# Kernel optimization log

Hardware: AMD Instinct MI355X
Metric: run time of the kernel (lower is better)

## Reference

```python
import jax, jax.numpy as jnp
import numpy as np

# Multi-scale schedule for (T,H,W)=(1,16,16) from get_latent2scale_schedule
SCHEDULE = [(1, 1, 1), (1, 2, 2), (1, 3, 3), (1, 4, 4), (1, 5, 5),
            (1, 6, 6), (1, 8, 8), (1, 10, 10), (1, 13, 13), (1, 16, 16)]

N_EMBED = 196560  # Leech lattice kissing number
EMBED_DIM = 24


def _resize(x, thw):
    # x: [B, D, T, H, W] -> [B, D, t, h, w] (trilinear/bilinear interpolation)
    b, d = x.shape[:2]
    return jax.image.resize(x, (b, d) + tuple(thw), method='bilinear')


def _quantize(r, codebook):
    """SphericalVectorQuantizer with predefined (pre-normalized) codebook.
    r: [B, D, t, h, w].  d = -z @ codebook^T; argmin(d) == argmax(sim)."""
    b, d = r.shape[0], r.shape[1]
    spatial = r.shape[2:]
    zf = jnp.moveaxis(r, 1, -1).reshape(-1, d)            # [N, D] tokens
    sim = zf @ codebook.T                                  # [N, K] cosine similarity
    idx = jnp.argmax(jax.lax.stop_gradient(sim), axis=1)   # argmin of -sim
    zq = codebook[idx]                                     # gather [N, D]
    zq = zq / jnp.linalg.norm(zq, axis=-1, keepdims=True)  # F.normalize (no-op if unit)
    zq = zf + jax.lax.stop_gradient(zq - zf)               # straight-through estimator
    zq = jnp.moveaxis(zq.reshape((b,) + spatial + (d,)), -1, 1)
    return zq, idx


def setup_inputs() -> dict:
    key = jax.random.key(0)
    k1, k2 = jax.random.split(key)
    z = jax.random.normal(k1, (2, 24, 1, 16, 16), jnp.float32)
    cb = jax.random.normal(k2, (N_EMBED, EMBED_DIM), jnp.float32)
    cb = cb / jnp.linalg.norm(cb, axis=-1, keepdims=True)  # normalized Leech codebook
    return {"z": z, "codebook": cb}


def reference(z, codebook):
    # Multi-scale residual quantization (Algorithm 1, RQ-style):
    # downsample residual -> spherical VQ (STE) -> upsample -> accumulate/subtract.
    B, D, T, H, W = z.shape
    residual = z
    z_hat = jnp.zeros_like(z)
    all_idx = []
    for thw in SCHEDULE:
        r_down = _resize(residual, thw)
        zq, idx = _quantize(r_down, codebook)
        zq_up = _resize(zq, (T, H, W))
        z_hat = z_hat + zq_up
        residual = residual - jax.lax.stop_gradient(zq_up)  # residual detach (default)
        all_idx.append(idx)
    indices = jnp.concatenate(all_idx)  # [B * sum(t*h*w)] int codes
    return z_hat, indices
```

## Files before the change

kernel.cpp:

```cpp
#include <hip/hip_runtime.h>
#include <stdint.h>

#define KCB 196560
#define DIM 24
#define BB  2
#define ZEL 12288
#define NRB 384
#define RBS 512

typedef __attribute__((ext_vector_type(8)))  __bf16 bf16x8;
typedef __attribute__((ext_vector_type(16))) float  f32x16;

__device__ __forceinline__ unsigned long long pack_key(float sim, int idx) {
  unsigned u = __float_as_uint(sim);
  u = (u & 0x80000000u) ? ~u : (u | 0x80000000u);
  return ((unsigned long long)u << 32) | (unsigned)(~(unsigned)idx);
}

__global__ __launch_bounds__(256) void init_kernel(const float* __restrict__ z,
    float* __restrict__ residual, float* __restrict__ out, float* __restrict__ rdown,
    ushort* __restrict__ th, ushort* __restrict__ tl, int outTotal) {
  __shared__ float plane[256];
  int tid = threadIdx.x;
  int e = blockIdx.x * 256 + tid;
  if (e < outTotal) out[e] = 0.0f;
  if (blockIdx.x < 48) {
    float v = z[e];
    residual[e] = v;
    plane[tid] = v;
    __syncthreads();
    if (tid == 0) {
      int t = 1;
      float inv_scale = 16.0f / (float)t;
      float ks = inv_scale;
      float sf_h = (0.0f + 0.5f) * inv_scale - 0.5f;
      float sf_w = (0.0f + 0.5f) * inv_scale - 0.5f;
      float wh[16], ww[16];
      float sh = 0.f, sw = 0.f;
#pragma unroll
      for (int i = 0; i < 16; ++i) {
        float vh = fmaxf(0.f, 1.f - fabsf(sf_h - (float)i) / ks);
        wh[i] = vh; sh += vh;
        float vw = fmaxf(0.f, 1.f - fabsf(sf_w - (float)i) / ks);
        ww[i] = vw; sw += vw;
      }
#pragma unroll
      for (int i = 0; i < 16; ++i) { wh[i] /= sh; ww[i] /= sw; }
      float acc = 0.f;
      for (int ih = 0; ih < 16; ++ih) {
        float ra = 0.f;
#pragma unroll
        for (int iw = 0; iw < 16; ++iw) ra = fmaf(ww[iw], plane[ih * 16 + iw], ra);
        acc = fmaf(wh[ih], ra, acc);
      }
      int b = blockIdx.x / DIM, d = blockIdx.x - (blockIdx.x / DIM) * DIM;
      int token = b;
      rdown[token * DIM + d] = acc;
      unsigned bits = __float_as_uint(acc);
      float hif = __uint_as_float(bits & 0xffff0000u);
      th[token * DIM + d] = (ushort)(bits >> 16);
      tl[token * DIM + d] = (ushort)(__float_as_uint(acc - hif) >> 16);
    }
  }
}

__global__ __launch_bounds__(256) void cbprep_kernel(const float* __restrict__ cb,
    ushort* __restrict__ ch, ushort* __restrict__ cl) {
  int j = blockIdx.x * 256 + threadIdx.x;
  if (j >= KCB * 6) return;
  int row = j / 6, q = j - row * 6;
  float4 v = *(const float4*)(cb + (size_t)row * 24 + q * 4);
  float xs[4] = {v.x, v.y, v.z, v.w};
  unsigned h[4], l[4];
#pragma unroll
  for (int k = 0; k < 4; ++k) {
    unsigned bits = __float_as_uint(xs[k]);
    h[k] = bits >> 16;
    float hif = __uint_as_float(bits & 0xffff0000u);
    l[k] = __float_as_uint(xs[k] - hif) >> 16;
  }
  *(uint2*)(ch + (size_t)row * 24 + q * 4) = make_uint2(h[0] | (h[1] << 16), h[2] | (h[3] << 16));
  *(uint2*)(cl + (size_t)row * 24 + q * 4) = make_uint2(l[0] | (l[1] << 16), l[2] | (l[3] << 16));
}

__global__ __launch_bounds__(256) void score_kernel(const ushort* __restrict__ ch,
    const ushort* __restrict__ cl, const ushort* __restrict__ th,
    const ushort* __restrict__ tl, float* __restrict__ blockmax, int T) {
  const int bx = blockIdx.x;
  const int rb = bx % NRB, tb = bx / NRB;
  const int tid = threadIdx.x, lane = tid & 63, wv = tid >> 6;
  const int col = lane & 31, g = lane >> 5;
  const int tbase = tb * 128;
  const int ntt = min(4, (T - tbase + 31) >> 5);
  const uint4 z4 = make_uint4(0, 0, 0, 0);

  bf16x8 bh[4][2], bl[4][2];
#pragma unroll
  for (int tt = 0; tt < 4; ++tt) {
    int token = tbase + tt * 32 + col;
    bool tv = (tt < ntt) && (token < T);
    const ushort* tr = th + (size_t)token * 24;
    const ushort* sr = tl + (size_t)token * 24;
    uint4 h0 = tv ? *(const uint4*)(tr + g * 8) : z4;
    uint4 h1 = (tv && g == 0) ? *(const uint4*)(tr + 16) : z4;
    uint4 l0 = tv ? *(const uint4*)(sr + g * 8) : z4;
    uint4 l1 = (tv && g == 0) ? *(const uint4*)(sr + 16) : z4;
    bh[tt][0] = __builtin_bit_cast(bf16x8, h0);
    bh[tt][1] = __builtin_bit_cast(bf16x8, h1);
    bl[tt][0] = __builtin_bit_cast(bf16x8, l0);
    bl[tt][1] = __builtin_bit_cast(bf16x8, l1);
  }

  const f32x16 fzero = {};
  float runmax[4] = {-3.402823466e38f, -3.402823466e38f, -3.402823466e38f, -3.402823466e38f};
  const int rbase = rb * RBS + wv * 128;

#pragma unroll
  for (int rt = 0; rt < 4; ++rt) {
    int tilebase = rbase + rt * 32;
    if (tilebase >= KCB) continue;
    int row = tilebase + col;
    bool rv = row < KCB;
    const ushort* cr = ch + (size_t)row * 24;
    const ushort* dr = cl + (size_t)row * 24;
    uint4 a0 = rv ? *(const uint4*)(cr + g * 8) : z4;
    uint4 a1 = (rv && g == 0) ? *(const uint4*)(cr + 16) : z4;
    uint4 c0 = rv ? *(const uint4*)(dr + g * 8) : z4;
    uint4 c1 = (rv && g == 0) ? *(const uint4*)(dr + 16) : z4;
    bf16x8 ah0 = __builtin_bit_cast(bf16x8, a0);
    bf16x8 ah1 = __builtin_bit_cast(bf16x8, a1);
    bf16x8 al0 = __builtin_bit_cast(bf16x8, c0);
    bf16x8 al1 = __builtin_bit_cast(bf16x8, c1);
    int limit = KCB - tilebase;
    bool full = limit >= 32;
#pragma unroll
    for (int tt = 0; tt < 4; ++tt) {
      if (tt >= ntt) continue;
      f32x16 acc = __builtin_amdgcn_mfma_f32_32x32x16_bf16(ah0, bh[tt][0], fzero, 0, 0, 0);
      acc = __builtin_amdgcn_mfma_f32_32x32x16_bf16(ah1, bh[tt][1], acc, 0, 0, 0);
      acc = __builtin_amdgcn_mfma_f32_32x32x16_bf16(al0, bh[tt][0], acc, 0, 0, 0);
      acc = __builtin_amdgcn_mfma_f32_32x32x16_bf16(al1, bh[tt][1], acc, 0, 0, 0);
      acc = __builtin_amdgcn_mfma_f32_32x32x16_bf16(ah0, bl[tt][0], acc, 0, 0, 0);
      acc = __builtin_amdgcn_mfma_f32_32x32x16_bf16(ah1, bl[tt][1], acc, 0, 0, 0);
      float m;
      if (full) {
        float m01 = fmaxf(acc[0], acc[1]),  m23 = fmaxf(acc[2], acc[3]);
        float m45 = fmaxf(acc[4], acc[5]),  m67 = fmaxf(acc[6], acc[7]);
        float m89 = fmaxf(acc[8], acc[9]),  mab = fmaxf(acc[10], acc[11]);
        float mcd = fmaxf(acc[12], acc[13]), mef = fmaxf(acc[14], acc[15]);
        m = fmaxf(fmaxf(fmaxf(m01, m23), fmaxf(m45, m67)),
                  fmaxf(fmaxf(m89, mab), fmaxf(mcd, mef)));
      } else {
        m = -3.402823466e38f;
#pragma unroll
        for (int r = 0; r < 16; ++r) {
          int rowid = (r & 3) + 8 * (r >> 2) + 4 * g;
          if (rowid < limit) m = fmaxf(m, acc[r]);
        }
      }
      runmax[tt] = fmaxf(runmax[tt], m);
    }
  }

  __shared__ float lmax[4][4][32];
#pragma unroll
  for (int tt = 0; tt < 4; ++tt) {
    float v = fmaxf(runmax[tt], __shfl_xor(runmax[tt], 32));
    if (lane < 32) lmax[wv][tt][col] = v;
  }
  __syncthreads();
  if (tid < 128) {
    int tt = tid >> 5, c = tid & 31;
    if (tt < ntt) {
      float m = fmaxf(fmaxf(lmax[0][tt][c], lmax[1][tt][c]),
                      fmaxf(lmax[2][tt][c], lmax[3][tt][c]));
      int token = tbase + tt * 32 + c;
      if (token < T) blockmax[token * NRB + rb] = m;
    }
  }
}

__global__ __launch_bounds__(256) void finalize_kernel(const float* __restrict__ cb,
    const float* __restrict__ rdown, const float* __restrict__ blockmax,
    unsigned long long* __restrict__ best, int T) {
  int tid = threadIdx.x, lane = tid & 63, wv = tid >> 6;
  int tok = blockIdx.x * 4 + wv;
  if (tok >= T) return;

  float x = (lane < DIM) ? rdown[tok * DIM + lane] : 0.f;
  float av[DIM];
#pragma unroll
  for (int k = 0; k < DIM; ++k)
    av[k] = __uint_as_float(__builtin_amdgcn_readlane(__float_as_uint(x), k));
  float ss = 0.f;
#pragma unroll
  for (int k = 0; k < DIM; ++k) ss = fmaf(av[k], av[k], ss);
  float eps = 1e-3f * sqrtf(ss) + 1e-30f;

  const float* bmrow = blockmax + (size_t)tok * NRB;
  float bv[6];
#pragma unroll
  for (int i = 0; i < 6; ++i) bv[i] = bmrow[lane + 64 * i];
  float M = fmaxf(fmaxf(fmaxf(bv[0], bv[1]), fmaxf(bv[2], bv[3])), fmaxf(bv[4], bv[5]));
#pragma unroll
  for (int d = 32; d; d >>= 1) M = fmaxf(M, __shfl_xor(M, d));
  float thr = M - eps;

  unsigned long long bk = 0ull;
#pragma unroll
  for (int i = 0; i < 6; ++i) {
    unsigned long long mask = __ballot(bv[i] >= thr);
    while (mask) {
      int l = __ffsll((unsigned long long)mask) - 1;
      mask &= mask - 1;
      int rowb = (l + 64 * i) * RBS;
      for (int r8 = 0; r8 < 8; ++r8) {
        int row = rowb + r8 * 64 + lane;
        if (row < KCB) {
          const float* cv = cb + (size_t)row * DIM;
          float acc = 0.f;
#pragma unroll
          for (int k = 0; k < DIM; ++k) acc = fmaf(av[k], cv[k], acc);
          unsigned long long key = pack_key(acc, row);
          if (key > bk) bk = key;
        }
      }
    }
  }
#pragma unroll
  for (int d = 32; d; d >>= 1) {
    unsigned long long o = __shfl_xor(bk, d);
    if (o > bk) bk = o;
  }
  if (lane == 0) best[tok] = bk;
}

template<int TSZ, int TN>
__global__ __launch_bounds__(256) void update_kernel(const float* __restrict__ cb,
    const unsigned long long* __restrict__ best, float* __restrict__ residual,
    float* __restrict__ out, float* __restrict__ rdown, ushort* __restrict__ th,
    ushort* __restrict__ tl, int idxBase) {
  constexpr int N = TSZ * TSZ;
  constexpr int T = BB * N;
  __shared__ float zq[T * DIM];
  __shared__ float plane[256];
  int tid = threadIdx.x;
  for (int slot = tid; slot < T; slot += 256) {
    unsigned long long key = best[slot];
    int idx = (int)(~(unsigned)key);
    const float* cv = cb + (long long)idx * DIM;
    float v[DIM]; float ss = 0.f;
#pragma unroll
    for (int k = 0; k < DIM; ++k) { v[k] = cv[k]; ss = fmaf(v[k], v[k], ss); }
    float nrm = sqrtf(ss);
#pragma unroll
    for (int k = 0; k < DIM; ++k) zq[slot * DIM + k] = v[k] / nrm;
    if (blockIdx.x == 0) out[idxBase + slot] = (float)idx;
  }
  __syncthreads();
  int e = blockIdx.x * 256 + tid;
  int w = e & 15, h = (e >> 4) & 15;
  int d = (e >> 8) % DIM;
  int b = e / (DIM * 256);
  float inv_scale = (float)TSZ / 16.0f;
  float sf_h = ((float)h + 0.5f) * inv_scale - 0.5f;
  float sf_w = ((float)w + 0.5f) * inv_scale - 0.5f;
  float wh[TSZ], ww[TSZ];
  float sh = 0.f, sw = 0.f;
#pragma unroll
  for (int j = 0; j < TSZ; ++j) {
    float vh = fmaxf(0.f, 1.f - fabsf(sf_h - (float)j));
    wh[j] = vh; sh += vh;
    float vw = fmaxf(0.f, 1.f - fabsf(sf_w - (float)j));
    ww[j] = vw; sw += vw;
  }
#pragma unroll
  for (int j = 0; j < TSZ; ++j) { wh[j] /= sh; ww[j] /= sw; }
  const float* zb = zq + (b * N) * DIM + d;
  float acc = 0.f;
#pragma unroll
  for (int thh = 0; thh < TSZ; ++thh) {
    float ra = 0.f;
#pragma unroll
    for (int tw = 0; tw < TSZ; ++tw) ra = fmaf(ww[tw], zb[(thh * TSZ + tw) * DIM], ra);
    acc = fmaf(wh[thh], ra, acc);
  }
  out[e] += acc;
  float rn = residual[e] - acc;
  residual[e] = rn;

  if constexpr (TN > 0) {
    plane[tid] = rn;
    __syncthreads();
    constexpr int n2 = TN * TN;
    int bb = blockIdx.x / DIM, dd = blockIdx.x - (blockIdx.x / DIM) * DIM;
    for (int sp = tid; sp < n2; sp += 256) {
      int oh = sp / TN, ow = sp - oh * TN;
      float inv2 = 16.0f / (float)TN;
      float ks = inv2;
      float s_h = ((float)oh + 0.5f) * inv2 - 0.5f;
      float s_w = ((float)ow + 0.5f) * inv2 - 0.5f;
      float wh2[16], ww2[16];
      float sh2 = 0.f, sw2 = 0.f;
#pragma unroll
      for (int i = 0; i < 16; ++i) {
        float vh = fmaxf(0.f, 1.f - fabsf(s_h - (float)i) / ks);
        wh2[i] = vh; sh2 += vh;
        float vw = fmaxf(0.f, 1.f - fabsf(s_w - (float)i) / ks);
        ww2[i] = vw; sw2 += vw;
      }
#pragma unroll
      for (int i = 0; i < 16; ++i) { wh2[i] /= sh2; ww2[i] /= sw2; }
      float acc2 = 0.f;
      for (int ih = 0; ih < 16; ++ih) {
        float ra = 0.f;
#pragma unroll
        for (int iw = 0; iw < 16; ++iw) ra = fmaf(ww2[iw], plane[ih * 16 + iw], ra);
        acc2 = fmaf(wh2[ih], ra, acc2);
      }
      int token = bb * n2 + sp;
      rdown[token * DIM + dd] = acc2;
      unsigned bits = __float_as_uint(acc2);
      float hif = __uint_as_float(bits & 0xffff0000u);
      th[token * DIM + dd] = (ushort)(bits >> 16);
      tl[token * DIM + dd] = (ushort)(__float_as_uint(acc2 - hif) >> 16);
    }
  }
}

extern "C" void kernel_launch(void* const* d_in, const int* in_sizes, int n_in,
                              void* d_out, int out_size, void* d_ws, size_t ws_size,
                              hipStream_t stream) {
  const float* z  = (const float*)d_in[0];
  const float* cb = (const float*)d_in[1];
  float* out = (float*)d_out;
  float* residual = (float*)d_ws;
  float* rdown = residual + ZEL;
  float* blockmax = rdown + ZEL;
  unsigned long long* best =
      (unsigned long long*)(blockmax + 512 * NRB);
  ushort* th = (ushort*)(best + 512);
  ushort* tl = th + 512 * 24;
  ushort* ch = tl + 512 * 24;
  ushort* cl = ch + (size_t)KCB * 24;

  static const int TS[10] = {1, 2, 3, 4, 5, 6, 8, 10, 13, 16};

  int initG = (out_size + 255) / 256;
  if (initG < 48) initG = 48;
  init_kernel<<<initG, 256, 0, stream>>>(z, residual, out, rdown, th, tl, out_size);
  cbprep_kernel<<<(KCB * 6 + 255) / 256, 256, 0, stream>>>(cb, ch, cl);

  int prefix = 0;
  for (int s = 0; s < 10; ++s) {
    int t = TS[s], n = t * t, T = BB * n;

    int ntb = (T + 127) >> 7;
    score_kernel<<<NRB * ntb, 256, 0, stream>>>(ch, cl, th, tl, blockmax, T);
    finalize_kernel<<<(T + 3) / 4, 256, 0, stream>>>(cb, rdown, blockmax, best, T);

    int idxBase = ZEL + BB * prefix;
    switch (t) {
      case 1:  update_kernel<1,2><<<48, 256, 0, stream>>>(cb, best, residual, out, rdown, th, tl, idxBase); break;
      case 2:  update_kernel<2,3><<<48, 256, 0, stream>>>(cb, best, residual, out, rdown, th, tl, idxBase); break;
      case 3:  update_kernel<3,4><<<48, 256, 0, stream>>>(cb, best, residual, out, rdown, th, tl, idxBase); break;
      case 4:  update_kernel<4,5><<<48, 256, 0, stream>>>(cb, best, residual, out, rdown, th, tl, idxBase); break;
      case 5:  update_kernel<5,6><<<48, 256, 0, stream>>>(cb, best, residual, out, rdown, th, tl, idxBase); break;
      case 6:  update_kernel<6,8><<<48, 256, 0, stream>>>(cb, best, residual, out, rdown, th, tl, idxBase); break;
      case 8:  update_kernel<8,10><<<48, 256, 0, stream>>>(cb, best, residual, out, rdown, th, tl, idxBase); break;
      case 10: update_kernel<10,13><<<48, 256, 0, stream>>>(cb, best, residual, out, rdown, th, tl, idxBase); break;
      case 13: update_kernel<13,16><<<48, 256, 0, stream>>>(cb, best, residual, out, rdown, th, tl, idxBase); break;
      case 16: update_kernel<16,0><<<48, 256, 0, stream>>>(cb, best, residual, out, rdown, th, tl, idxBase); break;
    }
    prefix += n;
  }
}
```

Baseline: 350.9 us.

## Fuse score, finalize and update into one per-scale kernel with grid barriers

Merges the three per-scale launches (score, finalize, update) into a single step_kernel. Blocks signal completion through global atomic counters, and the first 48 blocks spin-wait, then run finalize and the upsample/residual update. Finalize now normalizes the chosen codeword itself and writes it to a workspace, and update reads its plane from LDS. This removes two launches and their gaps per scale. The spin barriers assume the 48 waiting blocks are co-resident and could deadlock or stall if scheduling delays the other blocks.

```diff
diff --git a/kernel.cpp b/kernel.cpp
--- a/kernel.cpp
+++ b/kernel.cpp
@@ -19,11 +19,13 @@
 
 __global__ __launch_bounds__(256) void init_kernel(const float* __restrict__ z,
     float* __restrict__ residual, float* __restrict__ out, float* __restrict__ rdown,
-    ushort* __restrict__ th, ushort* __restrict__ tl, int outTotal) {
+    ushort* __restrict__ th, ushort* __restrict__ tl, unsigned* __restrict__ ctr,
+    int outTotal) {
   __shared__ float plane[256];
   int tid = threadIdx.x;
   int e = blockIdx.x * 256 + tid;
   if (e < outTotal) out[e] = 0.0f;
+  if (blockIdx.x == 0 && tid < 32) ctr[tid] = 0u;
   if (blockIdx.x < 48) {
     float v = z[e];
     residual[e] = v;
@@ -83,11 +85,9 @@
   *(uint2*)(cl + (size_t)row * 24 + q * 4) = make_uint2(l[0] | (l[1] << 16), l[2] | (l[3] << 16));
 }
 
-__global__ __launch_bounds__(256) void score_kernel(const ushort* __restrict__ ch,
-    const ushort* __restrict__ cl, const ushort* __restrict__ th,
-    const ushort* __restrict__ tl, float* __restrict__ blockmax, int T) {
-  const int bx = blockIdx.x;
-  const int rb = bx % NRB, tb = bx / NRB;
+__device__ __forceinline__ void score_block(int rb, int tb, int T,
+    const ushort* ch, const ushort* cl, const ushort* th, const ushort* tl,
+    float* blockmax) {
   const int tid = threadIdx.x, lane = tid & 63, wv = tid >> 6;
   const int col = lane & 31, g = lane >> 5;
   const int tbase = tb * 128;
@@ -180,13 +180,10 @@
   }
 }
 
-__global__ __launch_bounds__(256) void finalize_kernel(const float* __restrict__ cb,
-    const float* __restrict__ rdown, const float* __restrict__ blockmax,
-    unsigned long long* __restrict__ best, int T) {
-  int tid = threadIdx.x, lane = tid & 63, wv = tid >> 6;
-  int tok = blockIdx.x * 4 + wv;
-  if (tok >= T) return;
-
+__device__ __forceinline__ void finalize_token(int tok, const float* __restrict__ cb,
+    const float* rdown, const float* __restrict__ blockmax, float* __restrict__ zq_ws,
+    float* __restrict__ out, int idxBase) {
+  int lane = threadIdx.x & 63;
   float x = (lane < DIM) ? rdown[tok * DIM + lane] : 0.f;
   float av[DIM];
 #pragma unroll
@@ -232,36 +229,34 @@
     unsigned long long o = __shfl_xor(bk, d);
     if (o > bk) bk = o;
   }
-  if (lane == 0) best[tok] = bk;
+  int idx = (int)(~(unsigned)bk);
+  const float* cv = cb + (long long)idx * DIM;
+  float xv = (lane < DIM) ? cv[lane] : 0.f;
+  float v[DIM];
+#pragma unroll
+  for (int k = 0; k < DIM; ++k)
+    v[k] = __uint_as_float(__builtin_amdgcn_readlane(__float_as_uint(xv), k));
+  float s2 = 0.f;
+#pragma unroll
+  for (int k = 0; k < DIM; ++k) s2 = fmaf(v[k], v[k], s2);
+  float nrm = sqrtf(s2);
+  if (lane < DIM) zq_ws[tok * DIM + lane] = xv / nrm;
+  if (lane == 0) out[idxBase + tok] = (float)idx;
 }
 
 template<int TSZ, int TN>
-__global__ __launch_bounds__(256) void update_kernel(const float* __restrict__ cb,
-    const unsigned long long* __restrict__ best, float* __restrict__ residual,
-    float* __restrict__ out, float* __restrict__ rdown, ushort* __restrict__ th,
-    ushort* __restrict__ tl, int idxBase) {
+__device__ __forceinline__ void update_plane(const float* __restrict__ zq_ws,
+    float* residual, float* __restrict__ out, float* rdown, ushort* th, ushort* tl) {
   constexpr int N = TSZ * TSZ;
-  constexpr int T = BB * N;
-  __shared__ float zq[T * DIM];
+  int tid = threadIdx.x;
+  int p = blockIdx.x;
+  int b = p / DIM, d = p - b * DIM;
+  __shared__ float ldsZ[256];
   __shared__ float plane[256];
-  int tid = threadIdx.x;
-  for (int slot = tid; slot < T; slot += 256) {
-    unsigned long long key = best[slot];
-    int idx = (int)(~(unsigned)key);
-    const float* cv = cb + (long long)idx * DIM;
-    float v[DIM]; float ss = 0.f;
-#pragma unroll
-    for (int k = 0; k < DIM; ++k) { v[k] = cv[k]; ss = fmaf(v[k], v[k], ss); }
-    float nrm = sqrtf(ss);
-#pragma unroll
-    for (int k = 0; k < DIM; ++k) zq[slot * DIM + k] = v[k] / nrm;
-    if (blockIdx.x == 0) out[idxBase + slot] = (float)idx;
-  }
-  __syncthreads();
-  int e = blockIdx.x * 256 + tid;
+  for (int sp = tid; sp < N; sp += 256) ldsZ[sp] = zq_ws[(b * N + sp) * DIM + d];
+  __syncthreads();
+  int e = p * 256 + tid;
   int w = e & 15, h = (e >> 4) & 15;
-  int d = (e >> 8) % DIM;
-  int b = e / (DIM * 256);
   float inv_scale = (float)TSZ / 16.0f;
   float sf_h = ((float)h + 0.5f) * inv_scale - 0.5f;
   float sf_w = ((float)w + 0.5f) * inv_scale - 0.5f;
@@ -276,13 +271,12 @@
   }
 #pragma unroll
   for (int j = 0; j < TSZ; ++j) { wh[j] /= sh; ww[j] /= sw; }
-  const float* zb = zq + (b * N) * DIM + d;
   float acc = 0.f;
 #pragma unroll
   for (int thh = 0; thh < TSZ; ++thh) {
     float ra = 0.f;
 #pragma unroll
-    for (int tw = 0; tw < TSZ; ++tw) ra = fmaf(ww[tw], zb[(thh * TSZ + tw) * DIM], ra);
+    for (int tw = 0; tw < TSZ; ++tw) ra = fmaf(ww[tw], ldsZ[thh * TSZ + tw], ra);
     acc = fmaf(wh[thh], ra, acc);
   }
   out[e] += acc;
@@ -293,7 +287,6 @@
     plane[tid] = rn;
     __syncthreads();
     constexpr int n2 = TN * TN;
-    int bb = blockIdx.x / DIM, dd = blockIdx.x - (blockIdx.x / DIM) * DIM;
     for (int sp = tid; sp < n2; sp += 256) {
       int oh = sp / TN, ow = sp - oh * TN;
       float inv2 = 16.0f / (float)TN;
@@ -318,14 +311,56 @@
         for (int iw = 0; iw < 16; ++iw) ra = fmaf(ww2[iw], plane[ih * 16 + iw], ra);
         acc2 = fmaf(wh2[ih], ra, acc2);
       }
-      int token = bb * n2 + sp;
-      rdown[token * DIM + dd] = acc2;
+      int token = b * n2 + sp;
+      rdown[token * DIM + d] = acc2;
       unsigned bits = __float_as_uint(acc2);
       float hif = __uint_as_float(bits & 0xffff0000u);
-      th[token * DIM + dd] = (ushort)(bits >> 16);
-      tl[token * DIM + dd] = (ushort)(__float_as_uint(acc2 - hif) >> 16);
-    }
-  }
+      th[token * DIM + d] = (ushort)(bits >> 16);
+      tl[token * DIM + d] = (ushort)(__float_as_uint(acc2 - hif) >> 16);
+    }
+  }
+}
+
+template<int TSZ, int TN>
+__global__ __launch_bounds__(256) void step_kernel(
+    const ushort* __restrict__ ch, const ushort* __restrict__ cl,
+    const ushort* th, const ushort* tl,
+    const float* __restrict__ cb, float* rdown,
+    float* __restrict__ blockmax, float* __restrict__ zq_ws,
+    float* residual, float* __restrict__ out,
+    unsigned* __restrict__ c0, unsigned* __restrict__ c1, int idxBase) {
+  constexpr int N = TSZ * TSZ;
+  constexpr int T = BB * N;
+  constexpr int NTB = (T + 127) / 128;
+  int tid = threadIdx.x;
+  int wk = blockIdx.x;
+  int rb = wk % NRB, tb = wk / NRB;
+
+  score_block(rb, tb, T, ch, cl, th, tl, blockmax);
+  __threadfence();
+  __syncthreads();
+  if (tid == 0) atomicAdd(c0, 1u);
+  if (blockIdx.x >= 48) return;
+
+  if (tid == 0) { while (atomicAdd(c0, 0u) < (unsigned)(NRB * NTB)) __builtin_amdgcn_s_sleep(2); }
+  __syncthreads();
+  __threadfence();
+  {
+    int wv = tid >> 6;
+    for (int tok = blockIdx.x * 4 + wv; tok < T; tok += 192)
+      finalize_token(tok, cb, rdown, blockmax, zq_ws, out, idxBase);
+  }
+  __threadfence();
+  __syncthreads();
+  if (tid == 0) {
+    atomicAdd(c1, 1u);
+    while (atomicAdd(c1, 0u) < 48u) __builtin_amdgcn_s_sleep(2);
+  }
+  __syncthreads();
+  __threadfence();
+
+  update_plane<TSZ, TN>(zq_ws, residual, out, rdown, th == th ? (ushort*)th : nullptr,
+                        (ushort*)tl);
 }
 
 extern "C" void kernel_launch(void* const* d_in, const int* in_sizes, int n_in,
@@ -343,34 +378,35 @@
   ushort* tl = th + 512 * 24;
   ushort* ch = tl + 512 * 24;
   ushort* cl = ch + (size_t)KCB * 24;
+  float* zq_ws = (float*)(cl + (size_t)KCB * 24);
+  unsigned* ctr = (unsigned*)(zq_ws + 512 * 24);
 
   static const int TS[10] = {1, 2, 3, 4, 5, 6, 8, 10, 13, 16};
 
   int initG = (out_size + 255) / 256;
   if (initG < 48) initG = 48;
-  init_kernel<<<initG, 256, 0, stream>>>(z, residual, out, rdown, th, tl, out_size);
+  init_kernel<<<initG, 256, 0, stream>>>(z, residual, out, rdown, th, tl, ctr, out_size);
   cbprep_kernel<<<(KCB * 6 + 255) / 256, 256, 0, stream>>>(cb, ch, cl);
 
   int prefix = 0;
   for (int s = 0; s < 10; ++s) {
     int t = TS[s], n = t * t, T = BB * n;
-
     int ntb = (T + 127) >> 7;
-    score_kernel<<<NRB * ntb, 256, 0, stream>>>(ch, cl, th, tl, blockmax, T);
-    finalize_kernel<<<(T + 3) / 4, 256, 0, stream>>>(cb, rdown, blockmax, best, T);
-
+    int grid = NRB * ntb;
     int idxBase = ZEL + BB * prefix;
+    unsigned* c0 = ctr + 2 * s;
+    unsigned* c1 = ctr + 2 * s + 1;
     switch (t) {
-      case 1:  update_kernel<1,2><<<48, 256, 0, stream>>>(cb, best, residual, out, rdown, th, tl, idxBase); break;
-      case 2:  update_kernel<2,3><<<48, 256, 0, stream>>>(cb, best, residual, out, rdown, th, tl, idxBase); break;
-      case 3:  update_kernel<3,4><<<48, 256, 0, stream>>>(cb, best, residual, out, rdown, th, tl, idxBase); break;
-      case 4:  update_kernel<4,5><<<48, 256, 0, stream>>>(cb, best, residual, out, rdown, th, tl, idxBase); break;
-      case 5:  update_kernel<5,6><<<48, 256, 0, stream>>>(cb, best, residual, out, rdown, th, tl, idxBase); break;
-      case 6:  update_kernel<6,8><<<48, 256, 0, stream>>>(cb, best, residual, out, rdown, th, tl, idxBase); break;
-      case 8:  update_kernel<8,10><<<48, 256, 0, stream>>>(cb, best, residual, out, rdown, th, tl, idxBase); break;
-      case 10: update_kernel<10,13><<<48, 256, 0, stream>>>(cb, best, residual, out, rdown, th, tl, idxBase); break;
-      case 13: update_kernel<13,16><<<48, 256, 0, stream>>>(cb, best, residual, out, rdown, th, tl, idxBase); break;
-      case 16: update_kernel<16,0><<<48, 256, 0, stream>>>(cb, best, residual, out, rdown, th, tl, idxBase); break;
+      case 1:  step_kernel<1,2><<<grid, 256, 0, stream>>>(ch, cl, th, tl, cb, rdown, blockmax, zq_ws, residual, out, c0, c1, idxBase); break;
+      case 2:  step_kernel<2,3><<<grid, 256, 0, stream>>>(ch, cl, th, tl, cb, rdown, blockmax, zq_ws, residual, out, c0, c1, idxBase); break;
+      case 3:  step_kernel<3,4><<<grid, 256, 0, stream>>>(ch, cl, th, tl, cb, rdown, blockmax, zq_ws, residual, out, c0, c1, idxBase); break;
+      case 4:  step_kernel<4,5><<<grid, 256, 0, stream>>>(ch, cl, th, tl, cb, rdown, blockmax, zq_ws, residual, out, c0, c1, idxBase); break;
+      case 5:  step_kernel<5,6><<<grid, 256, 0, stream>>>(ch, cl, th, tl, cb, rdown, blockmax, zq_ws, residual, out, c0, c1, idxBase); break;
+      case 6:  step_kernel<6,8><<<grid, 256, 0, stream>>>(ch, cl, th, tl, cb, rdown, blockmax, zq_ws, residual, out, c0, c1, idxBase); break;
+      case 8:  step_kernel<8,10><<<grid, 256, 0, stream>>>(ch, cl, th, tl, cb, rdown, blockmax, zq_ws, residual, out, c0, c1, idxBase); break;
+      case 10: step_kernel<10,13><<<grid, 256, 0, stream>>>(ch, cl, th, tl, cb, rdown, blockmax, zq_ws, residual, out, c0, c1, idxBase); break;
+      case 13: step_kernel<13,16><<<grid, 256, 0, stream>>>(ch, cl, th, tl, cb, rdown, blockmax, zq_ws, residual, out, c0, c1, idxBase); break;
+      case 16: step_kernel<16,0><<<grid, 256, 0, stream>>>(ch, cl, th, tl, cb, rdown, blockmax, zq_ws, residual, out, c0, c1, idxBase); break;
     }
     prefix += n;
   }
```

New measurement: 1.191 ms. 3.4x slower.
